# Kernel optimization log

Hardware: AMD Instinct MI355X
Metric: run time of the kernel (lower is better)

## Reference

```python
import jax, jax.numpy as jnp
import numpy as np

B, T, U, E, P, C = 32, 4096, 1024, 512, 512, 4
LN_EPS = 1e-5


def setup_inputs() -> dict:
    key = jax.random.key(0)
    k = jax.random.split(key, 6)
    enc_out = jax.random.normal(k[0], (B, T, E), dtype=jnp.float32)
    pred_out = jax.random.normal(k[1], (B, U, P), dtype=jnp.float32)
    frame_label = jax.random.randint(k[2], (B, T), 0, C)
    frame_tlabel = jax.random.randint(k[3], (B, U), 0, C)
    # every emotion id appears in each sample's label list (dense [B, C])
    label = jnp.tile(jnp.arange(C), (B, 1))
    # LayerNorm params (torch defaults: weight=1, bias=0)
    norm_w = jnp.ones((E + P,), dtype=jnp.float32)
    norm_b = jnp.zeros((E + P,), dtype=jnp.float32)
    # Linear head params
    head_w = jax.random.normal(k[4], (C, E + P), dtype=jnp.float32) * 0.02
    head_b = jnp.zeros((C,), dtype=jnp.float32)
    return {
        "enc_out": enc_out, "pred_out": pred_out,
        "frame_label": frame_label, "frame_tlabel": frame_tlabel,
        "label": label,
        "norm_w": norm_w, "norm_b": norm_b,
        "head_w": head_w, "head_b": head_b,
    }


def _masked_mean(x, ids, n_cls):
    # x: [B, S, D]; ids: [B, S] -> per-class mean [B, C, D] via one-hot segment-sum
    onehot = (ids[:, :, None] == jnp.arange(n_cls)[None, None, :]).astype(x.dtype)  # [B,S,C]
    cnt = onehot.sum(axis=1)                                   # [B, C]
    summed = jnp.einsum('bsc,bsd->bcd', onehot, x)             # [B, C, D]
    return summed / jnp.maximum(cnt, 1.0)[..., None]


def reference(enc_out, pred_out, frame_label, frame_tlabel, label, norm_w, norm_b, head_w, head_b):
    n_cls = head_w.shape[0]
    enc_mean = _masked_mean(enc_out, frame_label, n_cls)    # [B, C, E]
    pred_mean = _masked_mean(pred_out, frame_tlabel, n_cls)  # [B, C, P]
    feat = jnp.concatenate([enc_mean, pred_mean], axis=-1)   # [B, C, E+P]
    # LayerNorm over last dim
    mu = feat.mean(axis=-1, keepdims=True)
    var = jnp.mean((feat - mu) ** 2, axis=-1, keepdims=True)
    feat_n = (feat - mu) / jnp.sqrt(var + LN_EPS) * norm_w + norm_b
    logits = jnp.einsum('bcd,nd->bcn', feat_n, head_w) + head_b  # [B, C, n_cls]
    logp = jax.nn.log_softmax(logits, axis=-1)
    # loss += -log_softmax(head(norm(cat)))[emo] for each emo in label[i]
    bb, ll = label.shape
    sel = logp[jnp.arange(bb)[:, None], label, label]  # [B, L]
    loss = -sel.sum() / (bb * ll)
    return loss
```

## Files before the change

kernel.cpp:

```cpp
#include <hip/hip_runtime.h>
#include <math.h>

#define C_CLS 4
#define D_HALF 512
#define D4 128
#define DFEAT 1024
#define BB 32

typedef float f4 __attribute__((ext_vector_type(4)));

__global__ void masked_sum_fused(const float* __restrict__ enc, const float* __restrict__ pred,
                                 const int* __restrict__ fl, const int* __restrict__ ftl,
                                 float* __restrict__ enc_part, float* __restrict__ pred_part,
                                 float* __restrict__ out,
                                 int T, int U, int SE, int SP) {
    int bid = blockIdx.x;
    if (bid == 0 && threadIdx.x == 0) out[0] = 0.0f;

    const float* x; const int* labels; float* partial;
    int Tlen, splits, b, s;
    if (bid < BB * SE) {
        x = enc; labels = fl; partial = enc_part; Tlen = T; splits = SE;
        b = bid / SE; s = bid % SE;
    } else {
        int idx = bid - BB * SE;
        x = pred; labels = ftl; partial = pred_part; Tlen = U; splits = SP;
        b = idx / SP; s = idx % SP;
    }
    int len = Tlen / splits;
    int t0 = s * len;
    int tx = threadIdx.x & 127;
    int ty = threadIdx.x >> 7;

    __shared__ int lab[256];
    const int* labg = labels + (size_t)b * Tlen + t0;
    for (int i = threadIdx.x; i < len; i += 256) lab[i] = labg[i];
    __syncthreads();

    const f4* x4 = (const f4*)x + ((size_t)b * Tlen + t0) * D4 + tx;
    f4 acc[C_CLS];
#pragma unroll
    for (int k = 0; k < C_CLS; k++) acc[k] = (f4){0.f, 0.f, 0.f, 0.f};

    int t = ty;
    for (; t + 2 < len; t += 4) {
        f4 v0 = __builtin_nontemporal_load(&x4[(size_t)t * D4]);
        f4 v1 = __builtin_nontemporal_load(&x4[(size_t)(t + 2) * D4]);
        int c0 = lab[t], c1 = lab[t + 2];
#pragma unroll
        for (int k = 0; k < C_CLS; k++) {
            acc[k] += v0 * (float)(c0 == k);
            acc[k] += v1 * (float)(c1 == k);
        }
    }
    for (; t < len; t += 2) {
        f4 v = __builtin_nontemporal_load(&x4[(size_t)t * D4]);
        int c = lab[t];
#pragma unroll
        for (int k = 0; k < C_CLS; k++) acc[k] += v * (float)(c == k);
    }

    __shared__ f4 cbuf[C_CLS][D4];
    if (ty == 1) {
#pragma unroll
        for (int k = 0; k < C_CLS; k++) cbuf[k][tx] = acc[k];
    }
    __syncthreads();
    if (ty == 0) {
        f4* o4 = (f4*)partial + (size_t)(b * splits + s) * C_CLS * D4 + tx;
#pragma unroll
        for (int k = 0; k < C_CLS; k++)
            o4[(size_t)k * D4] = acc[k] + cbuf[k][tx];
    }
}

__device__ __forceinline__ float blockReduceSum256(float v) {
    __shared__ float red[4];
#pragma unroll
    for (int off = 32; off > 0; off >>= 1) v += __shfl_down(v, off);
    int wid = threadIdx.x >> 6, lane = threadIdx.x & 63;
    __syncthreads();
    if (lane == 0) red[wid] = v;
    __syncthreads();
    return red[0] + red[1] + red[2] + red[3];
}

__global__ void finalize_loss_kernel(const float* __restrict__ enc_part,
                                     const float* __restrict__ pred_part,
                                     const int* __restrict__ fl, const int* __restrict__ ftl,
                                     const int* __restrict__ label,
                                     const float* __restrict__ norm_w, const float* __restrict__ norm_b,
                                     const float* __restrict__ head_w, const float* __restrict__ head_b,
                                     float* __restrict__ out,
                                     int T, int U, int B, int SE, int SP) {
    int b = blockIdx.x;
    int c = blockIdx.y;

    int ce = 0, cp = 0;
    {
        const int* p = fl + (size_t)b * T;
        for (int i = threadIdx.x; i < T; i += 256) ce += (p[i] == c);
        const int* q = ftl + (size_t)b * U;
        for (int i = threadIdx.x; i < U; i += 256) cp += (q[i] == c);
    }
    float cnt_e = fmaxf(blockReduceSum256((float)ce), 1.0f);
    float cnt_p = fmaxf(blockReduceSum256((float)cp), 1.0f);

    __shared__ float feat[DFEAT];
    for (int d = threadIdx.x; d < D_HALF; d += 256) {
        float s = 0.f;
        for (int sp = 0; sp < SE; sp++)
            s += enc_part[((size_t)(b * SE + sp) * C_CLS + c) * D_HALF + d];
        feat[d] = s / cnt_e;
    }
    for (int d = threadIdx.x; d < D_HALF; d += 256) {
        float s = 0.f;
        for (int sp = 0; sp < SP; sp++)
            s += pred_part[((size_t)(b * SP + sp) * C_CLS + c) * D_HALF + d];
        feat[D_HALF + d] = s / cnt_p;
    }
    __syncthreads();

    float lsum = 0.f;
    for (int d = threadIdx.x; d < DFEAT; d += 256) lsum += feat[d];
    float mu = blockReduceSum256(lsum) * (1.0f / DFEAT);

    float lvar = 0.f;
    for (int d = threadIdx.x; d < DFEAT; d += 256) {
        float t = feat[d] - mu;
        lvar = fmaf(t, t, lvar);
    }
    float var = blockReduceSum256(lvar) * (1.0f / DFEAT);
    float rstd = rsqrtf(var + 1e-5f);

    float part[C_CLS] = {0.f, 0.f, 0.f, 0.f};
    for (int d = threadIdx.x; d < DFEAT; d += 256) {
        float fn = (feat[d] - mu) * rstd * norm_w[d] + norm_b[d];
#pragma unroll
        for (int n = 0; n < C_CLS; n++)
            part[n] = fmaf(fn, head_w[(size_t)n * DFEAT + d], part[n]);
    }
    float logits[C_CLS];
#pragma unroll
    for (int n = 0; n < C_CLS; n++)
        logits[n] = blockReduceSum256(part[n]) + head_b[n];

    if (threadIdx.x == 0) {
        float m = fmaxf(fmaxf(logits[0], logits[1]), fmaxf(logits[2], logits[3]));
        float se = 0.f;
#pragma unroll
        for (int n = 0; n < C_CLS; n++) se += expf(logits[n] - m);
        float lp = logits[c] - (m + logf(se));
        int occ = 0;
#pragma unroll
        for (int l = 0; l < C_CLS; l++) occ += (label[b * C_CLS + l] == c);
        if (occ)
            atomicAdd(out, -lp * (float)occ * (1.0f / (BB * C_CLS)));
    }
}

extern "C" void kernel_launch(void* const* d_in, const int* in_sizes, int n_in,
                              void* d_out, int out_size, void* d_ws, size_t ws_size,
                              hipStream_t stream) {
    const float* enc_out      = (const float*)d_in[0];
    const float* pred_out     = (const float*)d_in[1];
    const int*   frame_label  = (const int*)d_in[2];
    const int*   frame_tlabel = (const int*)d_in[3];
    const int*   label        = (const int*)d_in[4];
    const float* norm_w       = (const float*)d_in[5];
    const float* norm_b       = (const float*)d_in[6];
    const float* head_w       = (const float*)d_in[7];
    const float* head_b       = (const float*)d_in[8];
    float* out = (float*)d_out;

    const int B = BB, T = 4096, U = 1024;
    int SE = 64, SP = 32;
    auto need = [&](int se, int sp) -> size_t {
        return ((size_t)B * se * C_CLS * D_HALF + (size_t)B * sp * C_CLS * D_HALF)
               * sizeof(float);
    };
    while (need(SE, SP) > ws_size && SE > 16) { SE >>= 1; if (SP > 4) SP >>= 1; }

    float* enc_part  = (float*)d_ws;
    float* pred_part = enc_part + (size_t)B * SE * C_CLS * D_HALF;

    masked_sum_fused<<<B * SE + B * SP, 256, 0, stream>>>(enc_out, pred_out,
                                                          frame_label, frame_tlabel,
                                                          enc_part, pred_part, out,
                                                          T, U, SE, SP);
    finalize_loss_kernel<<<dim3(B, C_CLS), 256, 0, stream>>>(enc_part, pred_part,
                                                             frame_label, frame_tlabel, label,
                                                             norm_w, norm_b, head_w, head_b,
                                                             out, T, U, B, SE, SP);
}
```

Measured before the change: 437.3 us.

## Halve split partials, deepen load unroll, and restructure finalize to one-element-per-thread

The masked-sum kernel now issues four nontemporal loads per iteration instead of two, and uses half as many time splits, so fewer partial buffers are written and read back. The finalize kernel moves to 512 threads, each owning one feature element per half. It packs both class counts into one integer reduction, computes mean and variance in a single fused pass, and reduces all four logits in one block reduction. This removes the shared feature buffer and several block-wide syncs. The single-pass variance formula is slightly less numerically robust, and fewer splits means fewer blocks in the streaming kernel.

```diff
diff --git a/kernel.cpp b/kernel.cpp
--- a/kernel.cpp
+++ b/kernel.cpp
@@ -21,11 +21,11 @@
     int Tlen, splits, b, s;
     if (bid < BB * SE) {
         x = enc; labels = fl; partial = enc_part; Tlen = T; splits = SE;
-        b = bid / SE; s = bid % SE;
+        b = bid / SE; s = bid - b * SE;
     } else {
         int idx = bid - BB * SE;
         x = pred; labels = ftl; partial = pred_part; Tlen = U; splits = SP;
-        b = idx / SP; s = idx % SP;
+        b = idx / SP; s = idx - b * SP;
     }
     int len = Tlen / splits;
     int t0 = s * len;
@@ -43,14 +43,18 @@
     for (int k = 0; k < C_CLS; k++) acc[k] = (f4){0.f, 0.f, 0.f, 0.f};
 
     int t = ty;
-    for (; t + 2 < len; t += 4) {
+    for (; t + 6 < len; t += 8) {
         f4 v0 = __builtin_nontemporal_load(&x4[(size_t)t * D4]);
         f4 v1 = __builtin_nontemporal_load(&x4[(size_t)(t + 2) * D4]);
-        int c0 = lab[t], c1 = lab[t + 2];
+        f4 v2 = __builtin_nontemporal_load(&x4[(size_t)(t + 4) * D4]);
+        f4 v3 = __builtin_nontemporal_load(&x4[(size_t)(t + 6) * D4]);
+        int c0 = lab[t], c1 = lab[t + 2], c2 = lab[t + 4], c3 = lab[t + 6];
 #pragma unroll
         for (int k = 0; k < C_CLS; k++) {
             acc[k] += v0 * (float)(c0 == k);
             acc[k] += v1 * (float)(c1 == k);
+            acc[k] += v2 * (float)(c2 == k);
+            acc[k] += v3 * (float)(c3 == k);
         }
     }
     for (; t < len; t += 2) {
@@ -74,78 +78,132 @@
     }
 }
 
-__device__ __forceinline__ float blockReduceSum256(float v) {
-    __shared__ float red[4];
-#pragma unroll
-    for (int off = 32; off > 0; off >>= 1) v += __shfl_down(v, off);
-    int wid = threadIdx.x >> 6, lane = threadIdx.x & 63;
-    __syncthreads();
-    if (lane == 0) red[wid] = v;
-    __syncthreads();
-    return red[0] + red[1] + red[2] + red[3];
-}
-
-__global__ void finalize_loss_kernel(const float* __restrict__ enc_part,
-                                     const float* __restrict__ pred_part,
-                                     const int* __restrict__ fl, const int* __restrict__ ftl,
-                                     const int* __restrict__ label,
-                                     const float* __restrict__ norm_w, const float* __restrict__ norm_b,
-                                     const float* __restrict__ head_w, const float* __restrict__ head_b,
-                                     float* __restrict__ out,
-                                     int T, int U, int B, int SE, int SP) {
+__device__ __forceinline__ float blockReduceSum512(float v) {
+    __shared__ float red[8];
+#pragma unroll
+    for (int off = 32; off; off >>= 1) v += __shfl_down(v, off);
+    int wid = threadIdx.x >> 6;
+    __syncthreads();
+    if ((threadIdx.x & 63) == 0) red[wid] = v;
+    __syncthreads();
+    float s = 0.f;
+#pragma unroll
+    for (int i = 0; i < 8; i++) s += red[i];
+    return s;
+}
+
+__device__ __forceinline__ void blockReduce2_512(float& a, float& b) {
+    __shared__ float red2[8][2];
+#pragma unroll
+    for (int off = 32; off; off >>= 1) {
+        a += __shfl_down(a, off);
+        b += __shfl_down(b, off);
+    }
+    int wid = threadIdx.x >> 6;
+    __syncthreads();
+    if ((threadIdx.x & 63) == 0) { red2[wid][0] = a; red2[wid][1] = b; }
+    __syncthreads();
+    float sa = 0.f, sb = 0.f;
+#pragma unroll
+    for (int i = 0; i < 8; i++) { sa += red2[i][0]; sb += red2[i][1]; }
+    a = sa; b = sb;
+}
+
+__device__ __forceinline__ void blockReduce4_512(float* p) {
+    __shared__ float red4[8][4];
+#pragma unroll
+    for (int off = 32; off; off >>= 1) {
+#pragma unroll
+        for (int n = 0; n < 4; n++) p[n] += __shfl_down(p[n], off);
+    }
+    int wid = threadIdx.x >> 6;
+    __syncthreads();
+    if ((threadIdx.x & 63) == 0) {
+#pragma unroll
+        for (int n = 0; n < 4; n++) red4[wid][n] = p[n];
+    }
+    __syncthreads();
+#pragma unroll
+    for (int n = 0; n < 4; n++) {
+        float s = 0.f;
+#pragma unroll
+        for (int i = 0; i < 8; i++) s += red4[i][n];
+        p[n] = s;
+    }
+}
+
+__global__ __launch_bounds__(512)
+void finalize_loss_kernel(const float* __restrict__ enc_part,
+                          const float* __restrict__ pred_part,
+                          const int* __restrict__ fl, const int* __restrict__ ftl,
+                          const int* __restrict__ label,
+                          const float* __restrict__ norm_w, const float* __restrict__ norm_b,
+                          const float* __restrict__ head_w, const float* __restrict__ head_b,
+                          float* __restrict__ out,
+                          int T, int U, int B, int SE, int SP) {
     int b = blockIdx.x;
     int c = blockIdx.y;
-
-    int ce = 0, cp = 0;
+    int d = threadIdx.x;
+
+    int pk = 0;
     {
         const int* p = fl + (size_t)b * T;
-        for (int i = threadIdx.x; i < T; i += 256) ce += (p[i] == c);
+        for (int i = d; i < T; i += 512) pk += (p[i] == c);
         const int* q = ftl + (size_t)b * U;
-        for (int i = threadIdx.x; i < U; i += 256) cp += (q[i] == c);
-    }
-    float cnt_e = fmaxf(blockReduceSum256((float)ce), 1.0f);
-    float cnt_p = fmaxf(blockReduceSum256((float)cp), 1.0f);
-
-    __shared__ float feat[DFEAT];
-    for (int d = threadIdx.x; d < D_HALF; d += 256) {
-        float s = 0.f;
-        for (int sp = 0; sp < SE; sp++)
-            s += enc_part[((size_t)(b * SE + sp) * C_CLS + c) * D_HALF + d];
-        feat[d] = s / cnt_e;
-    }
-    for (int d = threadIdx.x; d < D_HALF; d += 256) {
-        float s = 0.f;
-        for (int sp = 0; sp < SP; sp++)
-            s += pred_part[((size_t)(b * SP + sp) * C_CLS + c) * D_HALF + d];
-        feat[D_HALF + d] = s / cnt_p;
-    }
-    __syncthreads();
-
-    float lsum = 0.f;
-    for (int d = threadIdx.x; d < DFEAT; d += 256) lsum += feat[d];
-    float mu = blockReduceSum256(lsum) * (1.0f / DFEAT);
-
-    float lvar = 0.f;
-    for (int d = threadIdx.x; d < DFEAT; d += 256) {
-        float t = feat[d] - mu;
-        lvar = fmaf(t, t, lvar);
-    }
-    float var = blockReduceSum256(lvar) * (1.0f / DFEAT);
+        for (int i = d; i < U; i += 512) pk += (q[i] == c) << 13;
+    }
+
+    const int estr = C_CLS * D_HALF;
+    float e0 = 0.f, e1 = 0.f, e2 = 0.f, e3 = 0.f;
+    {
+        const float* ep = enc_part + ((size_t)b * SE * C_CLS + c) * D_HALF + d;
+        for (int sp = 0; sp < SE; sp += 4) {
+            e0 += ep[(size_t)(sp + 0) * estr];
+            e1 += ep[(size_t)(sp + 1) * estr];
+            e2 += ep[(size_t)(sp + 2) * estr];
+            e3 += ep[(size_t)(sp + 3) * estr];
+        }
+    }
+    float esum = (e0 + e1) + (e2 + e3);
+    float p0 = 0.f, p1 = 0.f, p2 = 0.f, p3 = 0.f;
+    {
+        const float* pp = pred_part + ((size_t)b * SP * C_CLS + c) * D_HALF + d;
+        for (int sp = 0; sp < SP; sp += 4) {
+            p0 += pp[(size_t)(sp + 0) * estr];
+            p1 += pp[(size_t)(sp + 1) * estr];
+            p2 += pp[(size_t)(sp + 2) * estr];
+            p3 += pp[(size_t)(sp + 3) * estr];
+        }
+    }
+    float psum = (p0 + p1) + (p2 + p3);
+
+    int cpk = (int)blockReduceSum512((float)pk);
+    float cnt_e = fmaxf((float)(cpk & 8191), 1.0f);
+    float cnt_p = fmaxf((float)(cpk >> 13), 1.0f);
+
+    float fe = esum / cnt_e;
+    float fp = psum / cnt_p;
+
+    float lsum = fe + fp;
+    float lsq  = fe * fe + fp * fp;
+    blockReduce2_512(lsum, lsq);
+    float mu   = lsum * (1.0f / DFEAT);
+    float var  = lsq * (1.0f / DFEAT) - mu * mu;
     float rstd = rsqrtf(var + 1e-5f);
 
-    float part[C_CLS] = {0.f, 0.f, 0.f, 0.f};
-    for (int d = threadIdx.x; d < DFEAT; d += 256) {
-        float fn = (feat[d] - mu) * rstd * norm_w[d] + norm_b[d];
-#pragma unroll
-        for (int n = 0; n < C_CLS; n++)
-            part[n] = fmaf(fn, head_w[(size_t)n * DFEAT + d], part[n]);
-    }
-    float logits[C_CLS];
+    float fn0 = (fe - mu) * rstd * norm_w[d] + norm_b[d];
+    float fn1 = (fp - mu) * rstd * norm_w[D_HALF + d] + norm_b[D_HALF + d];
+    float part[C_CLS];
 #pragma unroll
     for (int n = 0; n < C_CLS; n++)
-        logits[n] = blockReduceSum256(part[n]) + head_b[n];
+        part[n] = fn0 * head_w[(size_t)n * DFEAT + d]
+                + fn1 * head_w[(size_t)n * DFEAT + D_HALF + d];
+    blockReduce4_512(part);
 
     if (threadIdx.x == 0) {
+        float logits[C_CLS];
+#pragma unroll
+        for (int n = 0; n < C_CLS; n++) logits[n] = part[n] + head_b[n];
         float m = fmaxf(fmaxf(logits[0], logits[1]), fmaxf(logits[2], logits[3]));
         float se = 0.f;
 #pragma unroll
@@ -174,7 +232,7 @@
     float* out = (float*)d_out;
 
     const int B = BB, T = 4096, U = 1024;
-    int SE = 64, SP = 32;
+    int SE = 32, SP = 16;
     auto need = [&](int se, int sp) -> size_t {
         return ((size_t)B * se * C_CLS * D_HALF + (size_t)B * sp * C_CLS * D_HALF)
                * sizeof(float);
@@ -188,7 +246,7 @@
                                                           frame_label, frame_tlabel,
                                                           enc_part, pred_part, out,
                                                           T, U, SE, SP);
-    finalize_loss_kernel<<<dim3(B, C_CLS), 256, 0, stream>>>(enc_part, pred_part,
+    finalize_loss_kernel<<<dim3(B, C_CLS), 512, 0, stream>>>(enc_part, pred_part,
                                                              frame_label, frame_tlabel, label,
                                                              norm_w, norm_b, head_w, head_b,
                                                              out, T, U, B, SE, SP);
```

After: 390.7 us. -10.7%, faster.
